# Kernel optimization log

Measured on AMD Instinct MI355X. Metric: run time of the kernel, lower is better.

Reference implementation:

```python
import jax, jax.numpy as jnp
import numpy as np

EMBED_DIM = 768
NUM_HEADS = 12
HEAD_DIM = EMBED_DIM // NUM_HEADS


def setup_inputs() -> dict:
    key = jax.random.key(0)
    k_x, k_wqkv, k_bqkv, k_wo, k_bo = jax.random.split(key, 5)
    B, S, D = 4, 2048, EMBED_DIM
    bound = 1.0 / np.sqrt(D)
    x = jax.random.normal(k_x, (B, S, D), dtype=jnp.float32)
    # nn.Linear weights: torch stores [out, in]; we keep same layout and use x @ W.T
    W_qkv = jax.random.uniform(k_wqkv, (3 * D, D), jnp.float32, -bound, bound)
    b_qkv = jax.random.uniform(k_bqkv, (3 * D,), jnp.float32, -bound, bound)
    W_out = jax.random.uniform(k_wo, (D, D), jnp.float32, -bound, bound)
    b_out = jax.random.uniform(k_bo, (D,), jnp.float32, -bound, bound)
    return {"x": x, "W_qkv": W_qkv, "b_qkv": b_qkv, "W_out": W_out, "b_out": b_out}


def reference(x, W_qkv, b_qkv, W_out, b_out):
    B, S, D = x.shape
    H, Hd = NUM_HEADS, HEAD_DIM
    qkv = x @ W_qkv.T + b_qkv                       # [B,S,3D]
    qkv = qkv.reshape(B, S, H, 3 * Hd).transpose(0, 2, 1, 3)  # [B,H,S,3Hd]
    q, k, v = jnp.split(qkv, 3, axis=-1)            # each [B,H,S,Hd]
    scale = Hd ** -0.5
    scores = jnp.einsum("bhsd,bhtd->bhst", q, k) * scale  # [B,H,S,S]
    weights = jax.nn.softmax(scores, axis=-1)
    ctx = jnp.einsum("bhst,bhtd->bhsd", weights, v)       # [B,H,S,Hd]
    ctx = ctx.transpose(0, 2, 1, 3).reshape(B, S, D)      # [B,S,D]
    return ctx @ W_out.T + b_out
```

## Files before the change

### kernel.cpp

```cpp
#include <hip/hip_runtime.h>
#include <hip/hip_bf16.h>
#include <stdint.h>
#include <math.h>

typedef unsigned short u16;
typedef __attribute__((ext_vector_type(8))) short short8;
typedef __attribute__((ext_vector_type(4))) short short4v;
typedef __attribute__((ext_vector_type(4))) float f32x4;
typedef __attribute__((ext_vector_type(16))) float f32x16;
typedef __attribute__((ext_vector_type(4))) unsigned int u32x4;

#define NB 4
#define NS 2048
#define NH 12
#define HD 64
#define ND 768
#define ND3 2304

#define QSCALE 0.18033688f

__device__ __forceinline__ u16 f2bf(float f) {
    unsigned int u = __float_as_uint(f);
    unsigned int r = u + 0x7fffu + ((u >> 16) & 1u);
    return (u16)(r >> 16);
}

typedef const __attribute__((address_space(1))) unsigned int gu32;
typedef __attribute__((address_space(3))) unsigned int lu32;
__device__ __forceinline__ void async16(const void* g, void* l) {
    __builtin_amdgcn_global_load_lds((gu32*)(uintptr_t)g, (lu32*)(uintptr_t)l, 16, 0, 0);
}

#define XN4   1572864
#define WQN4  442368
#define WON4  147456
__global__ __launch_bounds__(256) void castall(const float* __restrict__ x,
                                               const float* __restrict__ wq,
                                               const float* __restrict__ wo,
                                               u16* __restrict__ xb,
                                               u16* __restrict__ wqb,
                                               u16* __restrict__ wob) {
    int i = blockIdx.x * 256 + threadIdx.x;
    const float* s; u16* d; int j;
    if (i < XN4) { s = x; d = xb; j = i; }
    else if (i < XN4 + WQN4) { s = wq; d = wqb; j = i - XN4; }
    else if (i < XN4 + WQN4 + WON4) { s = wo; d = wob; j = i - XN4 - WQN4; }
    else return;
    float4 v = ((const float4*)s)[j];
    ushort4 o;
    o.x = f2bf(v.x); o.y = f2bf(v.y); o.z = f2bf(v.z); o.w = f2bf(v.w);
    ((ushort4*)d)[j] = o;
}

__global__ __launch_bounds__(256, 3) void gemm_qkv(const u16* __restrict__ A,
                                                   const u16* __restrict__ Bw,
                                                   const float* __restrict__ bias,
                                                   u16* __restrict__ Qg,
                                                   u16* __restrict__ Kg,
                                                   u16* __restrict__ Vtg) {
    __shared__ u16 lds[10240];
    const int tid = threadIdx.x;
    const int w = tid >> 6, l = tid & 63;
    const int lam = l & 15, quad = l >> 4;
    const int wm = w >> 1, wn = w & 1;
    const int bm = blockIdx.x * 128;
    const int hh = blockIdx.y;
    const int bn = hh * 192;
    const int K = ND;

    f32x4 acc[4][6];
#pragma unroll
    for (int i = 0; i < 4; i++)
#pragma unroll
        for (int j = 0; j < 6; j++) { f32x4 z = {0.f, 0.f, 0.f, 0.f}; acc[i][j] = z; }

    const u16* gp[5];
    u16* sp[5];
#pragma unroll
    for (int i = 0; i < 5; i++) {
        int c = w * 5 + i;
        if (c < 8) { gp[i] = A + (size_t)(bm + c * 16 + lam) * K + quad * 8; sp[i] = lds + c * 512; }
        else { int nf = c - 8; gp[i] = Bw + (size_t)(bn + nf * 16 + lam) * K + quad * 8; sp[i] = lds + 4096 + nf * 512; }
    }

    for (int k0 = 0; k0 < K; k0 += 32) {
        __syncthreads();
#pragma unroll
        for (int i = 0; i < 5; i++) async16(gp[i] + k0, sp[i]);
        __syncthreads();
        short8 a[4];
#pragma unroll
        for (int i = 0; i < 4; i++) a[i] = *(const short8*)(lds + (wm * 4 + i) * 512 + l * 8);
#pragma unroll
        for (int half = 0; half < 2; half++) {
            short8 b[3];
#pragma unroll
            for (int j = 0; j < 3; j++) b[j] = *(const short8*)(lds + 4096 + (wn * 6 + half * 3 + j) * 512 + l * 8);
#pragma unroll
            for (int mf = 0; mf < 4; mf++)
#pragma unroll
                for (int j = 0; j < 3; j++)
                    acc[mf][half * 3 + j] = __builtin_amdgcn_mfma_f32_16x16x32_bf16(a[mf], b[j], acc[mf][half * 3 + j], 0, 0, 0);
        }
    }

#pragma unroll
    for (int nf = 0; nf < 6; nf++) {
        int nloc = wn * 96 + nf * 16;
        int rgn = nloc / 64;
        int d = (nloc % 64) + lam;
        float bv = bias[bn + nloc + lam];
        if (rgn == 2) {
#pragma unroll
            for (int mf = 0; mf < 4; mf++) {
                int m0 = bm + wm * 64 + mf * 16 + quad * 4;
                int bq = m0 >> 11, s0 = m0 & 2047;
                ushort4 o;
                o.x = f2bf(acc[mf][nf][0] + bv);
                o.y = f2bf(acc[mf][nf][1] + bv);
                o.z = f2bf(acc[mf][nf][2] + bv);
                o.w = f2bf(acc[mf][nf][3] + bv);
                *(ushort4*)(Vtg + ((size_t)((bq * NH + hh) * HD + d)) * NS + s0) = o;
            }
        } else {
            u16* dst = (rgn == 0) ? Qg : Kg;
            const float sc = (rgn == 0) ? QSCALE : 1.0f;
#pragma unroll
            for (int mf = 0; mf < 4; mf++)
#pragma unroll
                for (int r = 0; r < 4; r++) {
                    int m = bm + wm * 64 + mf * 16 + quad * 4 + r;
                    int bq = m >> 11, s = m & 2047;
                    dst[((size_t)((bq * NH + hh) * NS + s)) * HD + d] = f2bf((acc[mf][nf][r] + bv) * sc);
                }
        }
    }
}

__global__ __launch_bounds__(256, 3) void attn(const u16* __restrict__ Qg,
                                               const u16* __restrict__ Kg,
                                               const u16* __restrict__ Vtg,
                                               u16* __restrict__ ctx) {
    __shared__ u16 kt_lds[8192];
    __shared__ u16 vt_lds[8192];
    __shared__ float linv[128];
    const int tid = threadIdx.x;
    const int w = tid >> 6, L = tid & 63;
    const int r5 = L & 31, h = L >> 5;
    const int bid = blockIdx.x;
    const int qt = bid / 48, bh = bid % 48;
    const int b = bh / NH, hd = bh % NH;
    const u16* Qh = Qg + (size_t)bh * NS * HD;
    const u16* Kh = Kg + (size_t)bh * NS * HD;
    const u16* Vh = Vtg + (size_t)bh * HD * NS;

    const int qbase = qt * 128 + w * 32;

    short8 qf[4];
#pragma unroll
    for (int s = 0; s < 4; s++)
        qf[s] = *(const short8*)(Qh + (size_t)(qbase + r5) * HD + s * 16 + h * 8);

    f32x16 ot[2];
#pragma unroll
    for (int hg = 0; hg < 2; hg++)
#pragma unroll
        for (int r = 0; r < 16; r++) ot[hg][r] = 0.f;
    float lacc = 0.f;

    const u16* gp[8];
    u16* sp[8];
    int step;
    if (w < 2) {
#pragma unroll
        for (int i = 0; i < 8; i++) {
            int c = w * 8 + i, kg = c >> 2, s = c & 3;
            gp[i] = Kh + (size_t)(kg * 32 + r5) * HD + s * 16 + h * 8;
            sp[i] = kt_lds + c * 512;
        }
        step = 128 * HD;
    } else {
#pragma unroll
        for (int i = 0; i < 8; i++) {
            int c = (w - 2) * 8 + i;
            gp[i] = Vh + (size_t)((c >> 3) * 32 + r5) * NS + (c & 7) * 16 + h * 8;
            sp[i] = vt_lds + c * 512;
        }
        step = 128;
    }

    u32x4 rg[8];
#pragma unroll
    for (int i = 0; i < 8; i++) { rg[i] = *(const u32x4*)gp[i]; gp[i] += step; }

    for (int kt = 0; kt < 16; kt++) {
        __syncthreads();
#pragma unroll
        for (int i = 0; i < 8; i++) *(u32x4*)(sp[i] + (size_t)L * 8) = rg[i];
        __syncthreads();

        if (kt < 15) {
#pragma unroll
            for (int i = 0; i < 8; i++) { rg[i] = *(const u32x4*)gp[i]; gp[i] += step; }
        }

#pragma unroll
        for (int kg = 0; kg < 4; kg++) {
            f32x16 st;
#pragma unroll
            for (int r = 0; r < 16; r++) st[r] = 0.f;
#pragma unroll
            for (int s = 0; s < 4; s++) {
                short8 kf = *(const short8*)(kt_lds + (kg * 4 + s) * 512 + L * 8);
                st = __builtin_amdgcn_mfma_f32_32x32x16_bf16(kf, qf[s], st, 0, 0, 0);
            }

#pragma unroll
            for (int t4 = 0; t4 < 4; t4++) {
                float e0 = __builtin_amdgcn_exp2f(st[4 * t4 + 0]);
                float e1 = __builtin_amdgcn_exp2f(st[4 * t4 + 1]);
                float e2 = __builtin_amdgcn_exp2f(st[4 * t4 + 2]);
                float e3 = __builtin_amdgcn_exp2f(st[4 * t4 + 3]);
                lacc += (e0 + e1) + (e2 + e3);
                unsigned int u0 = __float_as_uint(e0) + 0x8000u;
                unsigned int u1 = __float_as_uint(e1) + 0x8000u;
                unsigned int u2 = __float_as_uint(e2) + 0x8000u;
                unsigned int u3 = __float_as_uint(e3) + 0x8000u;
                unsigned int pk0 = __builtin_amdgcn_perm(u1, u0, 0x07060302u);
                unsigned int pk1 = __builtin_amdgcn_perm(u3, u2, 0x07060302u);
                short4v pf;
                pf.x = (short)(pk0 & 0xffffu); pf.y = (short)(pk0 >> 16);
                pf.z = (short)(pk1 & 0xffffu); pf.w = (short)(pk1 >> 16);
                const int t = kg * 4 + t4;
#pragma unroll
                for (int hg = 0; hg < 2; hg++) {
                    short4v vf = *(const short4v*)(vt_lds + hg * 4096 + t * 256 + r5 * 8 + h * 4);
                    ot[hg] = __builtin_amdgcn_mfma_f32_32x32x8bf16_1k(pf, vf, ot[hg], 0, 0, 0);
                }
            }
        }
    }

    float lg = lacc + __shfl_xor(lacc, 32);
    linv[w * 32 + r5] = 1.0f / lg;
    __builtin_amdgcn_s_waitcnt(0xc07f);

    float sc[16];
#pragma unroll
    for (int r = 0; r < 16; r++) sc[r] = linv[w * 32 + (r & 3) + 8 * (r >> 2) + 4 * h];
#pragma unroll
    for (int hg = 0; hg < 2; hg++) {
#pragma unroll
        for (int r = 0; r < 16; r++) {
            int q = qbase + (r & 3) + 8 * (r >> 2) + 4 * h;
            ctx[(size_t)(b * NS + q) * ND + hd * HD + hg * 32 + r5] = f2bf(ot[hg][r] * sc[r]);
        }
    }
}

__global__ __launch_bounds__(256) void gemm_out(const u16* __restrict__ A,
                                                const u16* __restrict__ Bw,
                                                const float* __restrict__ bias,
                                                float* __restrict__ out) {
    __shared__ u16 lds[7168];
    const int tid = threadIdx.x;
    const int w = tid >> 6, l = tid & 63;
    const int lam = l & 15, quad = l >> 4;
    const int wm = w >> 1, wn = w & 1;
    const int bm = blockIdx.x * 128, bn = blockIdx.y * 96;
    const int K = ND;

    f32x4 acc[4][3];
#pragma unroll
    for (int i = 0; i < 4; i++)
#pragma unroll
        for (int j = 0; j < 3; j++) { f32x4 z = {0.f, 0.f, 0.f, 0.f}; acc[i][j] = z; }

    const u16* gp[4];
    u16* sp[4];
    int nact = 0;
#pragma unroll
    for (int i = 0; i < 4; i++) {
        int c = w * 4 + i;
        if (c < 8) { gp[nact] = A + (size_t)(bm + c * 16 + lam) * K + quad * 8; sp[nact] = lds + c * 512; nact++; }
        else if (c < 14) { int nf = c - 8; gp[nact] = Bw + (size_t)(bn + nf * 16 + lam) * K + quad * 8; sp[nact] = lds + 4096 + nf * 512; nact++; }
    }

    for (int k0 = 0; k0 < K; k0 += 32) {
        __syncthreads();
        for (int i = 0; i < nact; i++) async16(gp[i] + k0, sp[i]);
        __syncthreads();
        short8 a[4], b[3];
#pragma unroll
        for (int i = 0; i < 4; i++) a[i] = *(const short8*)(lds + (wm * 4 + i) * 512 + l * 8);
#pragma unroll
        for (int j = 0; j < 3; j++) b[j] = *(const short8*)(lds + 4096 + (wn * 3 + j) * 512 + l * 8);
#pragma unroll
        for (int mf = 0; mf < 4; mf++)
#pragma unroll
            for (int j = 0; j < 3; j++)
                acc[mf][j] = __builtin_amdgcn_mfma_f32_16x16x32_bf16(a[mf], b[j], acc[mf][j], 0, 0, 0);
    }

#pragma unroll
    for (int nf = 0; nf < 3; nf++) {
        int n = bn + wn * 48 + nf * 16 + lam;
        float bv = bias[n];
#pragma unroll
        for (int mf = 0; mf < 4; mf++)
#pragma unroll
            for (int r = 0; r < 4; r++) {
                int m = bm + wm * 64 + mf * 16 + quad * 4 + r;
                out[(size_t)m * ND + n] = acc[mf][nf][r] + bv;
            }
    }
}

extern "C" void kernel_launch(void* const* d_in, const int* in_sizes, int n_in,
                              void* d_out, int out_size, void* d_ws, size_t ws_size,
                              hipStream_t stream) {
    const float* x    = (const float*)d_in[0];
    const float* Wqkv = (const float*)d_in[1];
    const float* bqkv = (const float*)d_in[2];
    const float* Wout = (const float*)d_in[3];
    const float* bout = (const float*)d_in[4];
    float* out = (float*)d_out;

    u16* p = (u16*)d_ws;
    u16* xb    = p; p += 6291456;
    u16* wqkvb = p; p += 1769472;
    u16* wob   = p; p += 589824;
    u16* Qg    = p; p += 6291456;
    u16* Kg    = p; p += 6291456;
    u16* Vtg   = p; p += 6291456;
    u16* ctx   = p; p += 6291456;

    castall<<<8448, 256, 0, stream>>>(x, Wqkv, Wout, xb, wqkvb, wob);
    gemm_qkv<<<dim3(64, 12), 256, 0, stream>>>(xb, wqkvb, bqkv, Qg, Kg, Vtg);
    attn<<<768, 256, 0, stream>>>(Qg, Kg, Vtg, ctx);
    gemm_out<<<dim3(64, 8), 256, 0, stream>>>(ctx, wob, bout, out);
}
```

Before: 235.9 us.

## Register-prefetch GEMM tiles and use 32x32x16 MFMA for PV via permlane32 swap

```diff
diff --git a/kernel.cpp b/kernel.cpp
--- a/kernel.cpp
+++ b/kernel.cpp
@@ -9,6 +9,7 @@
 typedef __attribute__((ext_vector_type(4))) float f32x4;
 typedef __attribute__((ext_vector_type(16))) float f32x16;
 typedef __attribute__((ext_vector_type(4))) unsigned int u32x4;
+typedef __attribute__((ext_vector_type(2))) unsigned int u32x2;
 
 #define NB 4
 #define NS 2048
@@ -23,12 +24,6 @@
     unsigned int u = __float_as_uint(f);
     unsigned int r = u + 0x7fffu + ((u >> 16) & 1u);
     return (u16)(r >> 16);
-}
-
-typedef const __attribute__((address_space(1))) unsigned int gu32;
-typedef __attribute__((address_space(3))) unsigned int lu32;
-__device__ __forceinline__ void async16(const void* g, void* l) {
-    __builtin_amdgcn_global_load_lds((gu32*)(uintptr_t)g, (lu32*)(uintptr_t)l, 16, 0, 0);
 }
 
 #define XN4   1572864
@@ -83,11 +78,19 @@
         else { int nf = c - 8; gp[i] = Bw + (size_t)(bn + nf * 16 + lam) * K + quad * 8; sp[i] = lds + 4096 + nf * 512; }
     }
 
+    u32x4 rg[5];
+#pragma unroll
+    for (int i = 0; i < 5; i++) rg[i] = *(const u32x4*)gp[i];
+
     for (int k0 = 0; k0 < K; k0 += 32) {
         __syncthreads();
 #pragma unroll
-        for (int i = 0; i < 5; i++) async16(gp[i] + k0, sp[i]);
-        __syncthreads();
+        for (int i = 0; i < 5; i++) *(u32x4*)(sp[i] + (size_t)l * 8) = rg[i];
+        __syncthreads();
+        if (k0 + 32 < K) {
+#pragma unroll
+            for (int i = 0; i < 5; i++) rg[i] = *(const u32x4*)(gp[i] + k0 + 32);
+        }
         short8 a[4];
 #pragma unroll
         for (int i = 0; i < 4; i++) a[i] = *(const short8*)(lds + (wm * 4 + i) * 512 + l * 8);
@@ -215,28 +218,30 @@
                 st = __builtin_amdgcn_mfma_f32_32x32x16_bf16(kf, qf[s], st, 0, 0, 0);
             }
 
-#pragma unroll
-            for (int t4 = 0; t4 < 4; t4++) {
-                float e0 = __builtin_amdgcn_exp2f(st[4 * t4 + 0]);
-                float e1 = __builtin_amdgcn_exp2f(st[4 * t4 + 1]);
-                float e2 = __builtin_amdgcn_exp2f(st[4 * t4 + 2]);
-                float e3 = __builtin_amdgcn_exp2f(st[4 * t4 + 3]);
-                lacc += (e0 + e1) + (e2 + e3);
+            unsigned int q8[8];
+#pragma unroll
+            for (int i = 0; i < 8; i++) {
+                float e0 = __builtin_amdgcn_exp2f(st[2 * i + 0]);
+                float e1 = __builtin_amdgcn_exp2f(st[2 * i + 1]);
+                lacc += e0 + e1;
                 unsigned int u0 = __float_as_uint(e0) + 0x8000u;
                 unsigned int u1 = __float_as_uint(e1) + 0x8000u;
-                unsigned int u2 = __float_as_uint(e2) + 0x8000u;
-                unsigned int u3 = __float_as_uint(e3) + 0x8000u;
-                unsigned int pk0 = __builtin_amdgcn_perm(u1, u0, 0x07060302u);
-                unsigned int pk1 = __builtin_amdgcn_perm(u3, u2, 0x07060302u);
-                short4v pf;
-                pf.x = (short)(pk0 & 0xffffu); pf.y = (short)(pk0 >> 16);
-                pf.z = (short)(pk1 & 0xffffu); pf.w = (short)(pk1 >> 16);
-                const int t = kg * 4 + t4;
-#pragma unroll
-                for (int hg = 0; hg < 2; hg++) {
-                    short4v vf = *(const short4v*)(vt_lds + hg * 4096 + t * 256 + r5 * 8 + h * 4);
-                    ot[hg] = __builtin_amdgcn_mfma_f32_32x32x8bf16_1k(pf, vf, ot[hg], 0, 0, 0);
-                }
+                q8[i] = __builtin_amdgcn_perm(u1, u0, 0x07060302u);
+            }
+            u32x2 s02 = __builtin_amdgcn_permlane32_swap(q8[0], q8[2], false, false);
+            u32x2 s13 = __builtin_amdgcn_permlane32_swap(q8[1], q8[3], false, false);
+            u32x2 s46 = __builtin_amdgcn_permlane32_swap(q8[4], q8[6], false, false);
+            u32x2 s57 = __builtin_amdgcn_permlane32_swap(q8[5], q8[7], false, false);
+            union { u32x4 u; short8 s; } af0, af1;
+            af0.u = (u32x4){s02.x, s13.x, s02.y, s13.y};
+            af1.u = (u32x4){s46.x, s57.x, s46.y, s57.y};
+
+#pragma unroll
+            for (int hg = 0; hg < 2; hg++) {
+                short8 vf0 = *(const short8*)(vt_lds + (hg * 8 + kg * 2 + 0) * 512 + L * 8);
+                short8 vf1 = *(const short8*)(vt_lds + (hg * 8 + kg * 2 + 1) * 512 + L * 8);
+                ot[hg] = __builtin_amdgcn_mfma_f32_32x32x16_bf16(af0.s, vf0, ot[hg], 0, 0, 0);
+                ot[hg] = __builtin_amdgcn_mfma_f32_32x32x16_bf16(af1.s, vf1, ot[hg], 0, 0, 0);
             }
         }
     }
@@ -278,18 +283,27 @@
 
     const u16* gp[4];
     u16* sp[4];
-    int nact = 0;
 #pragma unroll
     for (int i = 0; i < 4; i++) {
         int c = w * 4 + i;
-        if (c < 8) { gp[nact] = A + (size_t)(bm + c * 16 + lam) * K + quad * 8; sp[nact] = lds + c * 512; nact++; }
-        else if (c < 14) { int nf = c - 8; gp[nact] = Bw + (size_t)(bn + nf * 16 + lam) * K + quad * 8; sp[nact] = lds + 4096 + nf * 512; nact++; }
-    }
+        if (c >= 14) c -= 14;
+        if (c < 8) { gp[i] = A + (size_t)(bm + c * 16 + lam) * K + quad * 8; sp[i] = lds + c * 512; }
+        else { int nf = c - 8; gp[i] = Bw + (size_t)(bn + nf * 16 + lam) * K + quad * 8; sp[i] = lds + 4096 + nf * 512; }
+    }
+
+    u32x4 rg[4];
+#pragma unroll
+    for (int i = 0; i < 4; i++) rg[i] = *(const u32x4*)gp[i];
 
     for (int k0 = 0; k0 < K; k0 += 32) {
         __syncthreads();
-        for (int i = 0; i < nact; i++) async16(gp[i] + k0, sp[i]);
-        __syncthreads();
+#pragma unroll
+        for (int i = 0; i < 4; i++) *(u32x4*)(sp[i] + (size_t)l * 8) = rg[i];
+        __syncthreads();
+        if (k0 + 32 < K) {
+#pragma unroll
+            for (int i = 0; i < 4; i++) rg[i] = *(const u32x4*)(gp[i] + k0 + 32);
+        }
         short8 a[4], b[3];
 #pragma unroll
         for (int i = 0; i < 4; i++) a[i] = *(const short8*)(lds + (wm * 4 + i) * 512 + l * 8);
```

New measurement: 232.3 us. No clear change (-1.5%).
